# Optimization experiments

Hardware: AMD Instinct MI355X
Metric: run time of the kernel (lower is better)

## Reference

```python
import jax, jax.numpy as jnp
import numpy as np

# ---- static configuration (mirrors ConvolutionConfig) ----
B_IMG, C_IN, H, W = 8, 16, 32, 32
C_OUT = 64
KH, KW = 5, 5          # receptive_field
SH, SW = 2, 2          # stride
PH, PW = 2, 2          # padding
N_BITS = 6             # n_inputs_per_node
HIDDEN = [36, 6, 1]    # 6^2, 6^1, 6^0 (tree_depth=2)
INPUT_SIZE = C_IN * KH * KW  # 400
OH = (H + 2 * PH - KH) // SH + 1  # 16
OW = (W + 2 * PW - KW) // SW + 1  # 16


def setup_inputs() -> dict:
    key = jax.random.key(0)
    ks = jax.random.split(key, 7)
    x = jax.random.uniform(ks[0], (B_IMG, C_IN, H, W), dtype=jnp.float32)
    # per-tree random input mappings (6 inputs per LUT node)
    idx0 = jax.random.randint(ks[1], (C_OUT, HIDDEN[0], N_BITS), 0, INPUT_SIZE)
    idx1 = jax.random.randint(ks[2], (C_OUT, HIDDEN[1], N_BITS), 0, HIDDEN[0])
    idx2 = jax.random.randint(ks[3], (C_OUT, HIDDEN[2], N_BITS), 0, HIDDEN[1])
    # raw LUT tables (64 entries), passed through sigmoid in forward
    table0 = jax.random.normal(ks[4], (C_OUT, HIDDEN[0], 64), dtype=jnp.float32)
    table1 = jax.random.normal(ks[5], (C_OUT, HIDDEN[1], 64), dtype=jnp.float32)
    table2 = jax.random.normal(ks[6], (C_OUT, HIDDEN[2], 64), dtype=jnp.float32)
    return {"x": x, "idx0": idx0, "table0": table0, "idx1": idx1,
            "table1": table1, "idx2": idx2, "table2": table2}


def _unfold(x):
    """torch nn.Unfold equivalent -> rows of [B*L, C*KH*KW], c slowest."""
    xp = jnp.pad(x, ((0, 0), (0, 0), (PH, PH), (PW, PW)))
    ri = (jnp.arange(OH) * SH)[:, None] + jnp.arange(KH)[None, :]  # [OH,KH]
    ci = (jnp.arange(OW) * SW)[:, None] + jnp.arange(KW)[None, :]  # [OW,KW]
    # [B, C, OH, OW, KH, KW]
    p = xp[:, :, ri[:, None, :, None], ci[None, :, None, :]]
    p = jnp.transpose(p, (0, 2, 3, 1, 4, 5))  # [B, OH, OW, C, KH, KW]
    return p.reshape(B_IMG * OH * OW, INPUT_SIZE)


def _lut_nodes(g, table):
    """Differentiable LUT node (multilinear interpolation over 2^6 table).
    g: [B, T, N, 6] probabilistic bits in [0,1]; table: [T, N, 64].
    Output: [B, T, N] = sum_a sigmoid(table)[a] * prod_i (g_i if bit_i(a) else 1-g_i).
    Computed by sequential bit contraction to avoid a [B,T,N,64] product tensor.
    """
    T, N = table.shape[0], table.shape[1]
    f = jnp.stack([1.0 - g, g], axis=-1)  # [B,T,N,6,2]
    w = jax.nn.sigmoid(table)             # [T,N,64]
    # contract most-significant bit first
    acc = jnp.einsum('tnkr,btnk->btnr', w.reshape(T, N, 2, 32), f[..., 0, :])
    for b in range(1, N_BITS):
        acc = jnp.einsum('btnkr,btnk->btnr',
                         acc.reshape(acc.shape[0], T, N, 2, -1), f[..., b, :])
    return acc[..., 0]  # [B,T,N]


def reference(x, idx0, table0, idx1, table1, idx2, table2):
    p = _unfold(x)                       # [BP, 400], BP = B*OH*OW
    tind = jnp.arange(C_OUT)[:, None, None]
    # first layer (chunked in torch; mathematically one big gathered layer)
    g0 = p[:, idx0]                      # [BP, C_OUT, 36, 6]
    h0 = _lut_nodes(g0, table0)          # [BP, C_OUT, 36]
    # tree layer 1: 36 -> 6 per tree
    g1 = h0[:, tind, idx1]               # [BP, C_OUT, 6, 6]
    h1 = _lut_nodes(g1, table1)          # [BP, C_OUT, 6]
    # tree layer 2: 6 -> 1 per tree
    g2 = h1[:, tind, idx2]               # [BP, C_OUT, 1, 6]
    h2 = _lut_nodes(g2, table2)[..., 0]  # [BP, C_OUT]
    out = h2.reshape(B_IMG, OH * OW, C_OUT)
    out = jnp.transpose(out, (0, 2, 1)).reshape(B_IMG, C_OUT, OH, OW)
    return out
```

## Files before the change

### kernel.cpp

```cpp
#include <hip/hip_runtime.h>
#include <hip/hip_fp16.h>

#define B_IMG 8
#define C_IN  16
#define COUT  64
#define H0    36
#define H1    6
#define NB    6
#define NNODE 43

typedef float f32x2 __attribute__((ext_vector_type(2)));
typedef float f32x4 __attribute__((ext_vector_type(4)));

__device__ __forceinline__ float sigf(float v) { return 1.0f / (1.0f + __expf(-v)); }
__device__ __forceinline__ float4 sig4(float4 a) {
    return make_float4(sigf(a.x), sigf(a.y), sigf(a.z), sigf(a.w));
}

__device__ __forceinline__ float lut_tree(const f32x4 lo[8], const f32x4 dd[8],
                                          const float g[NB]) {
    f32x4 v[8];
    const float g0 = g[0];
#pragma unroll
    for (int q = 0; q < 8; ++q) v[q] = lo[q] + dd[q] * g0;
    const float g1 = g[1], g2 = g[2], g3 = g[3];
#pragma unroll
    for (int q = 0; q < 4; ++q) v[q] += (v[q + 4] - v[q]) * g1;
#pragma unroll
    for (int q = 0; q < 2; ++q) v[q] += (v[q + 2] - v[q]) * g2;
    v[0] += (v[1] - v[0]) * g3;
    f32x2 a = {v[0].x, v[0].y};
    const f32x2 b = {v[0].z, v[0].w};
    a += (b - a) * g[4];
    return a.x + (a.y - a.x) * g[5];
}

__device__ __forceinline__ void load_tbl(const float* tb, f32x4 lo[8], f32x4 dd[8]) {
    const f32x4* t4 = (const f32x4*)tb;
#pragma unroll
    for (int q = 0; q < 8; ++q) { lo[q] = t4[q]; dd[q] = t4[q + 8]; }
}

__global__ __launch_bounds__(256) void lutone_kernel(
    const float* __restrict__ x,
    const int*   __restrict__ idx0,
    const float* __restrict__ t0,
    const int*   __restrict__ idx1,
    const float* __restrict__ t1,
    const int*   __restrict__ idx2,
    const float* __restrict__ t2,
    float*       __restrict__ out)
{
    __shared__ float  tblL[NNODE*64];
    __shared__ __half h0s[H0*256];
    __shared__ float  h1s[H1*256];
    __shared__ int    metaL[H0*NB*2];
    __shared__ int    idx1L[H1*NB];
    __shared__ int    idx2L[NB];

    const int tid  = threadIdx.x;
    const int w    = tid >> 6;
    const int lane = tid & 63;
    const int t    = blockIdx.x & 63;
    const int img  = blockIdx.x >> 6;

    {
        float4* tbl4 = (float4*)tblL;
        for (int e = tid; e < NNODE*8; e += 256) {
            const int node = e >> 3, q = e & 7;
            const float* src = (node < H0)      ? t0 + ((size_t)t*H0 + node)*64
                             : (node < H0+H1)   ? t1 + ((size_t)t*H1 + node - H0)*64
                                                : t2 + (size_t)t*64;
            const float4* s4 = (const float4*)src;
            const float4 lo = sig4(s4[q]);
            const float4 hi = sig4(s4[q + 8]);
            tbl4[node*16 + q]     = lo;
            tbl4[node*16 + 8 + q] = make_float4(hi.x - lo.x, hi.y - lo.y,
                                                hi.z - lo.z, hi.w - lo.w);
        }
    }
    if (tid < H0*NB) {
        const int raw = idx0[(size_t)t*(H0*NB) + tid];
        const int c2  = raw / 25;
        const int rem = raw - 25*c2;
        const int kh  = rem / 5, kw = rem - 5*kh;
        metaL[tid*2 + 0] = c2*1024 + kh*32 + kw - 66;
        metaL[tid*2 + 1] = rem;
    }
    if (tid < H1*NB) idx1L[tid] = idx1[(size_t)t*(H1*NB) + tid];
    if (tid < NB)    idx2L[tid] = idx2[(size_t)t*NB + tid];

    const int* i1base = idx1 + t*(H1*NB);
    unsigned long long umask = 0ull;
#pragma unroll
    for (int j = 0; j < H1*NB; ++j) umask |= 1ull << i1base[j];

    int base[4], vmask[4];
#pragma unroll
    for (int c = 0; c < 4; ++c) {
        const int p  = (c << 6) + lane;
        const int oh = p >> 4, ow = p & 15;
        base[c] = img*16384 + oh*64 + ow*2;
        const int hm = 0x1F ^ ((oh == 0) ? 0x03 : 0) ^ ((oh == 15) ? 0x10 : 0);
        const int wm = 0x1F ^ ((ow == 0) ? 0x03 : 0) ^ ((ow == 15) ? 0x10 : 0);
        int vm = 0;
#pragma unroll
        for (int kh = 0; kh < 5; ++kh)
            vm |= ((hm >> kh) & 1) ? (wm << (5*kh)) : 0;
        vmask[c] = vm;
    }

    int myn0=-1, myn1=-1, myn2=-1, myn3=-1, myn4=-1, myn5=-1, myn6=-1, myn7=-1, myn8=-1;
    {
        int cnt = 0;
        for (int n = 0; n < H0; ++n) {
            if (!((umask >> n) & 1ull)) continue;
            const int slot = cnt++;
            if ((slot & 3) != w) continue;
            switch (slot >> 2) {
                case 0: myn0 = n; break;
                case 1: myn1 = n; break;
                case 2: myn2 = n; break;
                case 3: myn3 = n; break;
                case 4: myn4 = n; break;
                case 5: myn5 = n; break;
                case 6: myn6 = n; break;
                case 7: myn7 = n; break;
                default: myn8 = n; break;
            }
        }
    }
    __syncthreads();

#define NODE_A(NN)                                                           \
    if ((NN) >= 0) {                                                         \
        const int4* mp = (const int4*)(metaL + (NN)*12);                     \
        const int4 ma = mp[0], mb = mp[1], mc = mp[2];                       \
        const int off_[NB] = {ma.x, ma.z, mb.x, mb.z, mc.x, mc.z};           \
        const int rem_[NB] = {ma.y, ma.w, mb.y, mb.w, mc.y, mc.w};           \
        f32x4 lo[8], dd[8];                                                  \
        load_tbl(tblL + (NN)*64, lo, dd);                                    \
        _Pragma("unroll")                                                    \
        for (int q = 0; q < 8; ++q)                                          \
            asm volatile("" : "+v"(lo[q]), "+v"(dd[q]));   \
        _Pragma("unroll")                                                    \
        for (int c = 0; c < 4; ++c) {                                        \
            float g[NB];                                                     \
            _Pragma("unroll")                                                \
            for (int i = 0; i < NB; ++i) {                                   \
                const bool ok = ((vmask[c] >> rem_[i]) & 1) != 0;            \
                const float v = x[ok ? (base[c] + off_[i]) : 0];             \
                g[i] = ok ? v : 0.0f;                                        \
            }                                                                \
            const float r = lut_tree(lo, dd, g);                             \
            h0s[(NN)*256 + (c << 6) + lane] = __float2half(r);               \
        }                                                                    \
    }
    NODE_A(myn0)
    NODE_A(myn1)
    NODE_A(myn2)
    NODE_A(myn3)
    NODE_A(myn4)
    NODE_A(myn5)
    NODE_A(myn6)
    NODE_A(myn7)
    NODE_A(myn8)
#undef NODE_A
    __syncthreads();

    {
#pragma unroll
        for (int n = 0; n < H1; ++n) {
            f32x4 lo[8], dd[8];
            load_tbl(tblL + (H0 + n)*64, lo, dd);
            const int* i1 = idx1L + n*NB;
            float g[NB];
#pragma unroll
            for (int i = 0; i < NB; ++i) g[i] = __half2float(h0s[i1[i]*256 + tid]);
            h1s[n*256 + tid] = lut_tree(lo, dd, g);
        }
    }
    __syncthreads();

    {
        f32x4 lo[8], dd[8];
        load_tbl(tblL + (H0 + H1)*64, lo, dd);
        float g[NB];
#pragma unroll
        for (int i = 0; i < NB; ++i) g[i] = h1s[idx2L[i]*256 + tid];
        out[((size_t)img*COUT + t)*256 + tid] = lut_tree(lo, dd, g);
    }
}

extern "C" void kernel_launch(void* const* d_in, const int* in_sizes, int n_in,
                              void* d_out, int out_size, void* d_ws, size_t ws_size,
                              hipStream_t stream) {
    const float* x      = (const float*)d_in[0];
    const int*   idx0   = (const int*)  d_in[1];
    const float* table0 = (const float*)d_in[2];
    const int*   idx1   = (const int*)  d_in[3];
    const float* table1 = (const float*)d_in[4];
    const int*   idx2   = (const int*)  d_in[5];
    const float* table2 = (const float*)d_in[6];
    float* out = (float*)d_out;

    lutone_kernel<<<COUT * B_IMG, 256, 0, stream>>>(
        x, idx0, table0, idx1, table1, idx2, table2, out);
}
```

Measured before the change: 25.28 us.

## Use 512-thread blocks, fp32 h0 storage, and register-resident tree tail

Doubles the block to 8 waves so the used first-layer nodes are spread over 8 waves instead of 4, and the table sigmoid setup runs in a single pass. First-layer outputs are stored as fp32 in shared memory instead of half. Layers 1 and 2 run on only the first 256 threads, with the 6 layer-1 results kept in registers and selected through a uniform select, which removes the h1 shared buffer and one barrier. This trades more LDS per block and half the threads idling in the tail for more parallelism in the dominant gather and LUT stage.

```diff
diff --git a/kernel.cpp b/kernel.cpp
--- a/kernel.cpp
+++ b/kernel.cpp
@@ -1,5 +1,4 @@
 #include <hip/hip_runtime.h>
-#include <hip/hip_fp16.h>
 
 #define B_IMG 8
 #define C_IN  16
@@ -41,7 +40,20 @@
     for (int q = 0; q < 8; ++q) { lo[q] = t4[q]; dd[q] = t4[q + 8]; }
 }
 
-__global__ __launch_bounds__(256) void lutone_kernel(
+__device__ __forceinline__ float sel6(const float h0_, const float h1_, const float h2_,
+                                      const float h3_, const float h4_, const float h5_,
+                                      int s) {
+    s = __builtin_amdgcn_readfirstlane(s);
+    float r = h0_;
+    r = (s == 1) ? h1_ : r;
+    r = (s == 2) ? h2_ : r;
+    r = (s == 3) ? h3_ : r;
+    r = (s == 4) ? h4_ : r;
+    r = (s == 5) ? h5_ : r;
+    return r;
+}
+
+__global__ __launch_bounds__(512) void lutone_kernel(
     const float* __restrict__ x,
     const int*   __restrict__ idx0,
     const float* __restrict__ t0,
@@ -51,12 +63,11 @@
     const float* __restrict__ t2,
     float*       __restrict__ out)
 {
-    __shared__ float  tblL[NNODE*64];
-    __shared__ __half h0s[H0*256];
-    __shared__ float  h1s[H1*256];
-    __shared__ int    metaL[H0*NB*2];
-    __shared__ int    idx1L[H1*NB];
-    __shared__ int    idx2L[NB];
+    __shared__ float tblL[NNODE*64];
+    __shared__ float h0s[H0*256];
+    __shared__ int   metaL[H0*NB*2];
+    __shared__ int   idx1L[H1*NB];
+    __shared__ int   idx2L[NB];
 
     const int tid  = threadIdx.x;
     const int w    = tid >> 6;
@@ -64,20 +75,18 @@
     const int t    = blockIdx.x & 63;
     const int img  = blockIdx.x >> 6;
 
-    {
+    if (tid < NNODE*8) {
+        const int node = tid >> 3, q = tid & 7;
+        const float* src = (node < H0)      ? t0 + ((size_t)t*H0 + node)*64
+                         : (node < H0+H1)   ? t1 + ((size_t)t*H1 + node - H0)*64
+                                            : t2 + (size_t)t*64;
+        const float4* s4 = (const float4*)src;
+        const float4 lo = sig4(s4[q]);
+        const float4 hi = sig4(s4[q + 8]);
         float4* tbl4 = (float4*)tblL;
-        for (int e = tid; e < NNODE*8; e += 256) {
-            const int node = e >> 3, q = e & 7;
-            const float* src = (node < H0)      ? t0 + ((size_t)t*H0 + node)*64
-                             : (node < H0+H1)   ? t1 + ((size_t)t*H1 + node - H0)*64
-                                                : t2 + (size_t)t*64;
-            const float4* s4 = (const float4*)src;
-            const float4 lo = sig4(s4[q]);
-            const float4 hi = sig4(s4[q + 8]);
-            tbl4[node*16 + q]     = lo;
-            tbl4[node*16 + 8 + q] = make_float4(hi.x - lo.x, hi.y - lo.y,
-                                                hi.z - lo.z, hi.w - lo.w);
-        }
+        tbl4[node*16 + q]     = lo;
+        tbl4[node*16 + 8 + q] = make_float4(hi.x - lo.x, hi.y - lo.y,
+                                            hi.z - lo.z, hi.w - lo.w);
     }
     if (tid < H0*NB) {
         const int raw = idx0[(size_t)t*(H0*NB) + tid];
@@ -110,24 +119,19 @@
         vmask[c] = vm;
     }
 
-    int myn0=-1, myn1=-1, myn2=-1, myn3=-1, myn4=-1, myn5=-1, myn6=-1, myn7=-1, myn8=-1;
+    int myn0 = -1, myn1 = -1, myn2 = -1, myn3 = -1, myn4 = -1;
     {
         int cnt = 0;
         for (int n = 0; n < H0; ++n) {
             if (!((umask >> n) & 1ull)) continue;
             const int slot = cnt++;
-            if ((slot & 3) != w) continue;
-            switch (slot >> 2) {
-                case 0: myn0 = n; break;
-                case 1: myn1 = n; break;
-                case 2: myn2 = n; break;
-                case 3: myn3 = n; break;
-                case 4: myn4 = n; break;
-                case 5: myn5 = n; break;
-                case 6: myn6 = n; break;
-                case 7: myn7 = n; break;
-                default: myn8 = n; break;
-            }
+            if ((slot & 7) != w) continue;
+            const int k = slot >> 3;
+            if      (k == 0) myn0 = n;
+            else if (k == 1) myn1 = n;
+            else if (k == 2) myn2 = n;
+            else if (k == 3) myn3 = n;
+            else             myn4 = n;
         }
     }
     __syncthreads();
@@ -142,7 +146,7 @@
         load_tbl(tblL + (NN)*64, lo, dd);                                    \
         _Pragma("unroll")                                                    \
         for (int q = 0; q < 8; ++q)                                          \
-            asm volatile("" : "+v"(lo[q]), "+v"(dd[q]));   \
+            asm volatile("" : "+v"(lo[q]), "+v"(dd[q]));                     \
         _Pragma("unroll")                                                    \
         for (int c = 0; c < 4; ++c) {                                        \
             float g[NB];                                                     \
@@ -152,8 +156,7 @@
                 const float v = x[ok ? (base[c] + off_[i]) : 0];             \
                 g[i] = ok ? v : 0.0f;                                        \
             }                                                                \
-            const float r = lut_tree(lo, dd, g);                             \
-            h0s[(NN)*256 + (c << 6) + lane] = __float2half(r);               \
+            h0s[(NN)*256 + (c << 6) + lane] = lut_tree(lo, dd, g);           \
         }                                                                    \
     }
     NODE_A(myn0)
@@ -161,33 +164,34 @@
     NODE_A(myn2)
     NODE_A(myn3)
     NODE_A(myn4)
-    NODE_A(myn5)
-    NODE_A(myn6)
-    NODE_A(myn7)
-    NODE_A(myn8)
 #undef NODE_A
     __syncthreads();
 
-    {
-#pragma unroll
-        for (int n = 0; n < H1; ++n) {
-            f32x4 lo[8], dd[8];
-            load_tbl(tblL + (H0 + n)*64, lo, dd);
-            const int* i1 = idx1L + n*NB;
-            float g[NB];
-#pragma unroll
-            for (int i = 0; i < NB; ++i) g[i] = __half2float(h0s[i1[i]*256 + tid]);
-            h1s[n*256 + tid] = lut_tree(lo, dd, g);
+    if (tid < 256) {
+        float h1v0, h1v1, h1v2, h1v3, h1v4, h1v5;
+#define NODE_B(N, DST)                                                       \
+        {                                                                    \
+            f32x4 lo[8], dd[8];                                              \
+            load_tbl(tblL + (H0 + (N))*64, lo, dd);                          \
+            const int* i1 = idx1L + (N)*NB;                                  \
+            float g[NB];                                                     \
+            _Pragma("unroll")                                                \
+            for (int i = 0; i < NB; ++i) g[i] = h0s[i1[i]*256 + tid];        \
+            DST = lut_tree(lo, dd, g);                                       \
         }
-    }
-    __syncthreads();
-
-    {
+        NODE_B(0, h1v0)
+        NODE_B(1, h1v1)
+        NODE_B(2, h1v2)
+        NODE_B(3, h1v3)
+        NODE_B(4, h1v4)
+        NODE_B(5, h1v5)
+#undef NODE_B
         f32x4 lo[8], dd[8];
         load_tbl(tblL + (H0 + H1)*64, lo, dd);
         float g[NB];
 #pragma unroll
-        for (int i = 0; i < NB; ++i) g[i] = h1s[idx2L[i]*256 + tid];
+        for (int i = 0; i < NB; ++i)
+            g[i] = sel6(h1v0, h1v1, h1v2, h1v3, h1v4, h1v5, idx2L[i]);
         out[((size_t)img*COUT + t)*256 + tid] = lut_tree(lo, dd, g);
     }
 }
@@ -204,6 +208,6 @@
     const float* table2 = (const float*)d_in[6];
     float* out = (float*)d_out;
 
-    lutone_kernel<<<COUT * B_IMG, 256, 0, stream>>>(
+    lutone_kernel<<<COUT * B_IMG, 512, 0, stream>>>(
         x, idx0, table0, idx1, table1, idx2, table2, out);
 }
```

New measurement: 26.91 us. 1.06x slower.
